# Optimization experiments

Hardware: AMD Instinct MI355X
Metric: run time of the kernel (lower is better)

## Reference

```python
import jax, jax.numpy as jnp
import numpy as np
import math

B, S, D = 2, 2048, 1024
H, HD = 16, 64
ROT = 16          # rotary_dim = head_dim * 0.25
FF = 4096
EPS = 1e-5


def setup_inputs() -> dict:
    key = jax.random.key(0)
    ks = jax.random.split(key, 12)
    sc = lambda *sh: 0.02
    inp = {
        "x": jax.random.normal(ks[0], (B, S, D), jnp.float32),
        "attention_mask": jnp.tril(jnp.ones((S, S), bool))[None, None],  # causal [1,1,S,S]
        "W_qkv": jax.random.normal(ks[1], (3 * D, D), jnp.float32) * 0.02,
        "b_qkv": jnp.zeros((3 * D,), jnp.float32),
        "W_o": jax.random.normal(ks[2], (D, D), jnp.float32) * 0.02,
        "b_o": jnp.zeros((D,), jnp.float32),
        "ln1_w": jnp.ones((D,), jnp.float32),
        "ln1_b": jnp.zeros((D,), jnp.float32),
        "ln2_w": jnp.ones((D,), jnp.float32),
        "ln2_b": jnp.zeros((D,), jnp.float32),
        "W1": jax.random.normal(ks[3], (FF, D), jnp.float32) * 0.02,
        "b1": jnp.zeros((FF,), jnp.float32),
        "W2": jax.random.normal(ks[4], (D, FF), jnp.float32) * 0.02,
        "b2": jnp.zeros((D,), jnp.float32),
    }
    # real rotary frequencies, shaped [1,1,S,ROT//2,2]
    inv_freq = 1.0 / (10000.0 ** (jnp.arange(0, ROT, 2, dtype=jnp.float32) / ROT))
    t = jnp.arange(S, dtype=jnp.float32)
    ang = t[:, None] * inv_freq[None, :]                      # [S, ROT//2]
    inp["freqs_cis"] = jnp.stack([jnp.cos(ang), jnp.sin(ang)], -1)[None, None]
    return inp


def layer_norm(x, w, b):
    mu = jnp.mean(x, -1, keepdims=True)
    var = jnp.mean(jnp.square(x - mu), -1, keepdims=True)
    return (x - mu) * jax.lax.rsqrt(var + EPS) * w + b


def apply_rotate_emb(x, freqs_cis):
    # x: [B,H,S,ROT]; freqs_cis: [1,1,S,ROT//2,2]
    x1, x2 = x[..., : ROT // 2], x[..., ROT // 2 :]
    cos, sin = freqs_cis[..., 0], freqs_cis[..., 1]
    return jnp.concatenate([x1 * cos - x2 * sin, x1 * sin + x2 * cos], -1)


def reference(x, attention_mask, freqs_cis, W_qkv, b_qkv, W_o, b_o,
              ln1_w, ln1_b, ln2_w, ln2_b, W1, b1, W2, b2):
    h = layer_norm(x, ln1_w, ln1_b)
    qkv = jnp.einsum("bsd,ed->bse", h, W_qkv) + b_qkv
    q, k, v = jnp.split(qkv, 3, axis=-1)
    to_heads = lambda t: t.reshape(B, S, H, HD).transpose(0, 2, 1, 3)  # [B,H,S,HD]
    q, k, v = to_heads(q), to_heads(k), to_heads(v)
    q = jnp.concatenate([apply_rotate_emb(q[..., :ROT], freqs_cis), q[..., ROT:]], -1)
    k = jnp.concatenate([apply_rotate_emb(k[..., :ROT], freqs_cis), k[..., ROT:]], -1)
    scores = jnp.einsum("bhqd,bhkd->bhqk", q, k) / math.sqrt(HD)
    scores = jnp.where(attention_mask, scores, -jnp.inf)
    probs = jax.nn.softmax(scores, axis=-1)
    out = jnp.einsum("bhqk,bhkd->bhqd", probs, v)
    out = out.transpose(0, 2, 1, 3).reshape(B, S, D)
    attn_out = jnp.einsum("bsd,ed->bse", out, W_o) + b_o
    # parallel residual (dropout is identity in eval)
    h2 = layer_norm(x, ln2_w, ln2_b)
    ff = jnp.einsum("bsf,df->bsd", jax.nn.gelu(jnp.einsum("bsd,fd->bsf", h2, W1) + b1, approximate=False), W2) + b2
    return x + ff + attn_out
```

## Files before the change

kernel.cpp:

```cpp
#include <hip/hip_runtime.h>

#define DEV __device__ __forceinline__

typedef __bf16 bf16;
typedef bf16 bf16x4 __attribute__((ext_vector_type(4)));
typedef bf16 bf16x8 __attribute__((ext_vector_type(8)));
typedef float f32x4 __attribute__((ext_vector_type(4)));

DEV f32x4 mfma16(bf16x8 a, bf16x8 b, f32x4 c) {
  return __builtin_amdgcn_mfma_f32_16x16x32_bf16(a, b, c, 0, 0, 0);
}

DEV void gload_lds16(const bf16* g, bf16* l) {
  __builtin_amdgcn_global_load_lds((const __attribute__((address_space(1))) void*)g,
                                   (__attribute__((address_space(3))) void*)l, 16, 0, 0);
}

#define PH_BAR __builtin_amdgcn_s_barrier()
#define VM(NSTR) asm volatile("s_waitcnt vmcnt(" NSTR ")" ::: "memory")
#define WAITBAR(NSTR) asm volatile("s_waitcnt vmcnt(" NSTR ")\n\ts_barrier" ::: "memory")

DEV float fast_gelu(float x) {
  const float z = x * x;
  const float w = __builtin_fmaf(z, 0.1029353f, 2.3019853f);
  const float e = __builtin_amdgcn_exp2f(x * w);
  const float r = __builtin_amdgcn_rcpf(1.0f + e);
  return x - x * r;
}

__global__ __launch_bounds__(256) void ln_cast_all(
    const float* __restrict__ x,
    const float* __restrict__ ln1w, const float* __restrict__ ln1b,
    const float* __restrict__ ln2w, const float* __restrict__ ln2b,
    bf16* __restrict__ h1, bf16* __restrict__ h2,
    const float* __restrict__ Wqkv_f, const float* __restrict__ W1_f,
    const float* __restrict__ Wo_f, const float* __restrict__ W2_f,
    bf16* __restrict__ wQKV, bf16* __restrict__ w1, bf16* __restrict__ wCat)
{
  const int b = blockIdx.x, t = threadIdx.x;
  if (b < 4096) {
    __shared__ float red[2][4];
    const int lane = t & 63, wave = t >> 6;
    const float4 v = ((const float4*)(x + (size_t)b * 1024))[t];
    float vv[4] = {v.x, v.y, v.z, v.w};
    float s = vv[0] + vv[1] + vv[2] + vv[3];
    float q = vv[0]*vv[0] + vv[1]*vv[1] + vv[2]*vv[2] + vv[3]*vv[3];
    #pragma unroll
    for (int o = 32; o; o >>= 1) { s += __shfl_xor(s, o); q += __shfl_xor(q, o); }
    if (lane == 0) { red[0][wave] = s; red[1][wave] = q; }
    __syncthreads();
    s = red[0][0] + red[0][1] + red[0][2] + red[0][3];
    q = red[1][0] + red[1][1] + red[1][2] + red[1][3];
    const float mu = s * (1.0f / 1024.0f);
    const float var = q * (1.0f / 1024.0f) - mu * mu;
    const float rs = rsqrtf(var + 1e-5f);
    bf16x4 o1, o2;
    #pragma unroll
    for (int j = 0; j < 4; ++j) {
      const int i = t * 4 + j;
      const float xh = (vv[j] - mu) * rs;
      o1[j] = (bf16)(xh * ln1w[i] + ln1b[i]);
      o2[j] = (bf16)(xh * ln2w[i] + ln2b[i]);
    }
    *(bf16x4*)&h1[(size_t)b * 1024 + t * 4] = o1;
    *(bf16x4*)&h2[(size_t)b * 1024 + t * 4] = o2;
    return;
  }
  const int cb = b - 4096;
  if (cb < 3072) {
    const int i = cb * 256 + t;
    const float4 v = ((const float4*)Wqkv_f)[i];
    bf16x4 o = {(bf16)v.x, (bf16)v.y, (bf16)v.z, (bf16)v.w};
    ((bf16x4*)wQKV)[i] = o;
  } else if (cb < 7168) {
    const int i = (cb - 3072) * 256 + t;
    const float4 v = ((const float4*)W1_f)[i];
    bf16x4 o = {(bf16)v.x, (bf16)v.y, (bf16)v.z, (bf16)v.w};
    ((bf16x4*)w1)[i] = o;
  } else if (cb < 8192) {
    const int row = cb - 7168;
    const float4 v = *(const float4*)&Wo_f[(size_t)row * 1024 + t * 4];
    bf16x4 o = {(bf16)v.x, (bf16)v.y, (bf16)v.z, (bf16)v.w};
    *(bf16x4*)&wCat[(size_t)row * 5120 + t * 4] = o;
  } else {
    const int row = cb - 8192;
    #pragma unroll
    for (int k = 0; k < 4; ++k) {
      const int col = t * 4 + k * 1024;
      const float4 v = *(const float4*)&W2_f[(size_t)row * 4096 + col];
      bf16x4 o = {(bf16)v.x, (bf16)v.y, (bf16)v.z, (bf16)v.w};
      *(bf16x4*)&wCat[(size_t)row * 5120 + 1024 + col] = o;
    }
  }
}

DEV bf16x8 ldfrag(const bf16* unit, int lr, int g) {
  return *(const bf16x8*)&unit[lr * 32 + ((g ^ ((lr >> 1) & 3)) << 3)];
}
DEV void read_bfr(const bf16* unit, int blr, int g, bf16x8 bfr[4]) {
  #pragma unroll
  for (int nj = 0; nj < 4; ++nj) bfr[nj] = ldfrag(unit, blr + nj * 16, g);
}
DEV void read_af(const bf16* unit, int alr, int g, bf16x8 af[4]) {
  #pragma unroll
  for (int ml = 0; ml < 4; ++ml) af[ml] = ldfrag(unit, alr + ml * 16, g);
}
DEV void do_mfma(const bf16x8 af[4], const bf16x8 bfr[4], f32x4 acc[8][4], int mh) {
  __builtin_amdgcn_s_setprio(1);
  #pragma unroll
  for (int ml = 0; ml < 4; ++ml)
    #pragma unroll
    for (int nj = 0; nj < 4; ++nj)
      acc[mh * 4 + ml][nj] = mfma16(af[ml], bfr[nj], acc[mh * 4 + ml][nj]);
  __builtin_amdgcn_s_setprio(0);
}

DEV void gemm_kloop(bf16 (*As)[2][2][4096], bf16 (*Bs)[2][2][4096],
                    const bf16* aU[2][2], const bf16* bU[2][2],
                    int wave, int alr, int blr, int bub, int g, int nkt,
                    f32x4 acc[8][4])
{
  bf16x8 bfr[4], af[4];
#define STG_A(bf_, kkh_, ub_, ko_) gload_lds16(aU[kkh_][ub_] + (ko_), &As[bf_][kkh_][ub_][wave * 512])
#define STG_B(bf_, kkh_, ub_, ko_) gload_lds16(bU[kkh_][ub_] + (ko_), &Bs[bf_][kkh_][ub_][wave * 512])
  STG_B(0, 0, 0, 0); STG_B(0, 0, 1, 0); STG_A(0, 0, 0, 0); STG_A(0, 0, 1, 0);
  STG_B(0, 1, 0, 0); STG_B(0, 1, 1, 0); STG_A(0, 1, 0, 0); STG_A(0, 1, 1, 0);
  WAITBAR("4");

  for (int t = 0; t < nkt - 1; ++t) {
    const int buf = t & 1, nxt = buf ^ 1;
    const int ko = (t + 1) * 64;
    read_bfr(&Bs[buf][0][bub][0], blr, g, bfr);
    read_af(&As[buf][0][0][0], alr, g, af);
    STG_B(nxt, 0, 0, ko); STG_B(nxt, 0, 1, ko);
    PH_BAR;
    do_mfma(af, bfr, acc, 0);
    PH_BAR;
    read_af(&As[buf][0][1][0], alr, g, af);
    STG_A(nxt, 0, 0, ko); STG_A(nxt, 0, 1, ko);
    PH_BAR;
    do_mfma(af, bfr, acc, 1);
    VM("4");
    PH_BAR;
    read_bfr(&Bs[buf][1][bub][0], blr, g, bfr);
    read_af(&As[buf][1][0][0], alr, g, af);
    STG_B(nxt, 1, 0, ko); STG_B(nxt, 1, 1, ko);
    PH_BAR;
    do_mfma(af, bfr, acc, 0);
    PH_BAR;
    read_af(&As[buf][1][1][0], alr, g, af);
    STG_A(nxt, 1, 0, ko); STG_A(nxt, 1, 1, ko);
    PH_BAR;
    do_mfma(af, bfr, acc, 1);
    VM("4");
    PH_BAR;
  }
  {
    const int buf = (nkt - 1) & 1;
    read_bfr(&Bs[buf][0][bub][0], blr, g, bfr);
    read_af(&As[buf][0][0][0], alr, g, af);
    PH_BAR;
    do_mfma(af, bfr, acc, 0);
    PH_BAR;
    read_af(&As[buf][0][1][0], alr, g, af);
    PH_BAR;
    do_mfma(af, bfr, acc, 1);
    VM("0");
    PH_BAR;
    read_bfr(&Bs[buf][1][bub][0], blr, g, bfr);
    read_af(&As[buf][1][0][0], alr, g, af);
    PH_BAR;
    do_mfma(af, bfr, acc, 0);
    PH_BAR;
    read_af(&As[buf][1][1][0], alr, g, af);
    PH_BAR;
    do_mfma(af, bfr, acc, 1);
  }
#undef STG_A
#undef STG_B
}

template <int EPI>
__global__ __launch_bounds__(512) void gemm256(
    const bf16* __restrict__ A, const bf16* __restrict__ B,
    const float* __restrict__ bias, void* __restrict__ Cv,
    void* __restrict__ P1, void* __restrict__ P2, void* __restrict__ P3,
    int K, int ldc, int ntiles, int nbx, int nkt)
{
  __shared__ __align__(16) bf16 As[2][2][2][4096];
  __shared__ __align__(16) bf16 Bs[2][2][2][4096];
  const int tid = threadIdx.x;
  const int lane = tid & 63, wave = tid >> 6;
  const int wm = wave >> 2, wn = wave & 3;
  const int g = lane >> 4, c = lane & 15;
  const int cpx = gridDim.x >> 3;
  const int swz = ((int)blockIdx.x & 7) * cpx + ((int)blockIdx.x >> 3);
  const int tile = swz % ntiles;
  const int sk = swz / ntiles;
  const int bm = (tile / nbx) * 256, bn = (tile % nbx) * 256;

  const int slr = tid >> 2;
  const int sch = (tid & 3) ^ ((tid >> 3) & 3);
  const bf16* aU[2][2];
  const bf16* bU[2][2];
  {
    const bf16* a0 = A + (size_t)(bm + ((slr >> 6) * 128) + (slr & 63)) * K
                       + (size_t)sk * nkt * 64 + sch * 8;
    const bf16* b0 = B + (size_t)(bn + slr) * K + (size_t)sk * nkt * 64 + sch * 8;
    aU[0][0] = a0;            aU[0][1] = a0 + (size_t)64 * K;
    aU[1][0] = a0 + 32;       aU[1][1] = a0 + (size_t)64 * K + 32;
    bU[0][0] = b0;            bU[0][1] = b0 + (size_t)128 * K;
    bU[1][0] = b0 + 32;       bU[1][1] = b0 + (size_t)128 * K + 32;
  }

  f32x4 acc[8][4] = {};
  const int alr = (wm << 6) + c;
  const int blr = ((wn & 1) << 6) + c;
  const int bub = wn >> 1;

  gemm_kloop(As, Bs, aU, bU, wave, alr, blr, bub, g, nkt, acc);

  bf16* Pp = nullptr;
  if constexpr (EPI == 2)
    Pp = (bf16*)((sk == 1) ? P1 : (sk == 2) ? P2 : (sk == 3) ? P3 : Cv);
  const int row0 = bm + wm * 128 + 4 * g;
  const int col0 = bn + wn * 64 + c;
  #pragma unroll
  for (int mi = 0; mi < 8; ++mi) {
    #pragma unroll
    for (int nj = 0; nj < 4; ++nj) {
      const int col = col0 + nj * 16;
      float bv = 0.0f;
      if constexpr (EPI < 2) bv = bias[col];
      #pragma unroll
      for (int r = 0; r < 4; ++r) {
        const size_t idx = (size_t)(row0 + mi * 16 + r) * ldc + col;
        float vo = acc[mi][nj][r] + bv;
        if constexpr (EPI == 0) {
          ((bf16*)Cv)[idx] = (bf16)vo;
        } else if constexpr (EPI == 1) {
          ((bf16*)Cv)[idx] = (bf16)fast_gelu(vo);
        } else {
          Pp[idx] = (bf16)vo;
        }
      }
    }
  }
}

__global__ __launch_bounds__(256) void combine_out(
    const bf16* __restrict__ q0, const bf16* __restrict__ q1,
    const bf16* __restrict__ q2, const bf16* __restrict__ q3,
    const float* __restrict__ x,
    const float* __restrict__ bo, const float* __restrict__ b2,
    float* __restrict__ out)
{
  const int row = blockIdx.x, t = threadIdx.x;
  const size_t base = (size_t)row * 1024 + t * 4;
  const bf16x4 a0 = *(const bf16x4*)&q0[base];
  const bf16x4 a1 = *(const bf16x4*)&q1[base];
  const bf16x4 a2 = *(const bf16x4*)&q2[base];
  const bf16x4 a3 = *(const bf16x4*)&q3[base];
  const float4 vx = *(const float4*)&x[base];
  const float4 vb = *(const float4*)&bo[t * 4];
  const float4 vc = *(const float4*)&b2[t * 4];
  float4 o;
  o.x = (float)a0[0] + (float)a1[0] + (float)a2[0] + (float)a3[0] + vx.x + vb.x + vc.x;
  o.y = (float)a0[1] + (float)a1[1] + (float)a2[1] + (float)a3[1] + vx.y + vb.y + vc.y;
  o.z = (float)a0[2] + (float)a1[2] + (float)a2[2] + (float)a3[2] + vx.z + vb.z + vc.z;
  o.w = (float)a0[3] + (float)a1[3] + (float)a2[3] + (float)a3[3] + vx.w + vb.w + vc.w;
  *(float4*)&out[base] = o;
}

__global__ __launch_bounds__(256) void rope_reshape(
    const bf16* __restrict__ qkv, const float* __restrict__ freqs,
    bf16* __restrict__ Q, bf16* __restrict__ K, bf16* __restrict__ VT)
{
  __shared__ bf16 vt[64][72];
  const int t = threadIdx.x;
  const int bh = blockIdx.y, b = bh >> 4, h = bh & 15;
  const int sc = blockIdx.x * 64;
  const int sl = t >> 2, s = sc + sl;
  const int d0 = (t & 3) * 16;

  const size_t rowbase = (size_t)(b * 2048 + s) * 3072 + h * 64 + d0;
  const size_t obase = ((size_t)bh * 2048 + s) * 64 + d0;

  #pragma unroll
  for (int which = 0; which < 2; ++which) {
    const bf16* src = qkv + rowbase + which * 1024;
    bf16x8 v0 = *(const bf16x8*)src;
    bf16x8 v1 = *(const bf16x8*)(src + 8);
    if (d0 == 0) {
      bf16x8 r0, r1;
      #pragma unroll
      for (int j = 0; j < 8; ++j) {
        const float cs = freqs[s * 16 + j * 2];
        const float sn = freqs[s * 16 + j * 2 + 1];
        const float x1 = (float)v0[j], x2 = (float)v1[j];
        r0[j] = (bf16)(x1 * cs - x2 * sn);
        r1[j] = (bf16)(x1 * sn + x2 * cs);
      }
      v0 = r0; v1 = r1;
    }
    bf16* dst = (which == 0 ? Q : K) + obase;
    *(bf16x8*)dst = v0;
    *(bf16x8*)(dst + 8) = v1;
  }
  {
    const bf16* src = qkv + rowbase + 2048;
    bf16x8 v0 = *(const bf16x8*)src;
    bf16x8 v1 = *(const bf16x8*)(src + 8);
    #pragma unroll
    for (int j = 0; j < 8; ++j) { vt[sl][d0 + j] = v0[j]; vt[sl][d0 + 8 + j] = v1[j]; }
  }
  __syncthreads();
  {
    const int d = t >> 2;
    const int s0 = (t & 3) * 16;
    bf16x8 o0, o1;
    #pragma unroll
    for (int j = 0; j < 8; ++j) { o0[j] = vt[s0 + j][d]; o1[j] = vt[s0 + 8 + j][d]; }
    bf16* dst = VT + ((size_t)bh * 64 + d) * 2048 + sc + s0;
    *(bf16x8*)dst = o0;
    *(bf16x8*)(dst + 8) = o1;
  }
}

__global__ __launch_bounds__(512, 4) void attn_kernel(
    const bf16* __restrict__ Q, const bf16* __restrict__ Kg,
    const bf16* __restrict__ VTg, bf16* __restrict__ O, int ldO)
{
  __shared__ __align__(16) bf16 Ks[4][64][64];
  __shared__ __align__(16) bf16 Vs[4][64][64];
  __shared__ __align__(16) bf16 Ps[8][16][64];

  const int tid = threadIdx.x;
  const int lane = tid & 63, wave = tid >> 6;
  const int g = lane >> 4, c = lane & 15;
  const int L = blockIdx.x;
  const int heavy = (L < 256);
  const int r = heavy ? L : (L - 256);
  const int bh = r >> 3;
  const int qtile = heavy ? (8 + (r & 7)) : (7 - (r & 7));
  const int qw = qtile * 128 + wave * 16;

  const bf16* Qp = Q + (size_t)bh * 2048 * 64;
  const bf16* Kp = Kg + (size_t)bh * 2048 * 64;
  const bf16* Vp = VTg + (size_t)bh * 64 * 2048;

  const int srow = lane >> 3;
  const int schunk = (lane & 7) ^ srow;
  const int svr = wave * 8 + srow;
  const size_t kdelta = (size_t)64 * 64;

  bf16x8 qreg[2];
  {
    const float qs = 0.125f * 1.44269504f;
    bf16x8 t0 = *(const bf16x8*)&Qp[(size_t)(qw + c) * 64 + g * 8];
    bf16x8 t1 = *(const bf16x8*)&Qp[(size_t)(qw + c) * 64 + 32 + g * 8];
    #pragma unroll
    for (int j = 0; j < 8; ++j) {
      qreg[0][j] = (bf16)((float)t0[j] * qs);
      qreg[1][j] = (bf16)((float)t1[j] * qs);
    }
  }
  bf16x8 ones;
  #pragma unroll
  for (int j = 0; j < 8; ++j) ones[j] = (bf16)1.0f;

  const int cq = c & 7;
  int fo[4][2];
  #pragma unroll
  for (int i = 0; i < 4; ++i)
    #pragma unroll
    for (int kk = 0; kk < 2; ++kk)
      fo[i][kk] = (i * 16 + c) * 64 + (((kk * 4 + g) ^ cq) << 3);
  bf16* pw[4];
  #pragma unroll
  for (int kf = 0; kf < 4; ++kf)
    pw[kf] = &Ps[wave][c][((((kf * 2 + (g >> 1)) ^ cq) << 3)) + ((g & 1) << 2)];
  const bf16* pr[2];
  #pragma unroll
  for (int kk = 0; kk < 2; ++kk)
    pr[kk] = &Ps[wave][c][((kk * 4 + g) ^ cq) << 3];
  const bf16* ks0 = &Ks[0][0][0];
  const bf16* vs0 = &Vs[0][0][0];

  f32x4 oacc[4] = {};
  f32x4 lacc = {};
  float m_ = -1e30f;

  const int nkb = 2 * qtile + 2;
#define STAGE(j_) do { const int b4_ = (j_) & 3;                                     \
    gload_lds16(&Kp[(size_t)((j_) * 64 + svr) * 64 + schunk * 8], &Ks[b4_][wave * 8][0]); \
    gload_lds16(&Vp[(size_t)svr * 2048 + (j_) * 64 + schunk * 8], &Vs[b4_][wave * 8][0]); \
  } while (0)

  auto qkt = [&](f32x4* st, int bufi) {
    const bf16* kt = ks0 + bufi * kdelta;
    __builtin_amdgcn_s_setprio(1);
    #pragma unroll
    for (int kf = 0; kf < 4; ++kf) {
      f32x4 z = {};
      z = mfma16(*(const bf16x8*)(kt + fo[kf][0]), qreg[0], z);
      st[kf] = mfma16(*(const bf16x8*)(kt + fo[kf][1]), qreg[1], z);
    }
    __builtin_amdgcn_s_setprio(0);
  };

  auto smpv = [&](const f32x4* st, int j_, int bufi) {
    const int kbase = j_ * 64;
    float v[16];
    if (kbase + 63 > qw) {
      const int qrel = qw + c - kbase;
      #pragma unroll
      for (int kf = 0; kf < 4; ++kf)
        #pragma unroll
        for (int rr = 0; rr < 4; ++rr)
          v[kf * 4 + rr] = (kf * 16 + 4 * g + rr <= qrel) ? st[kf][rr] : -1e30f;
    } else {
      #pragma unroll
      for (int kf = 0; kf < 4; ++kf)
        #pragma unroll
        for (int rr = 0; rr < 4; ++rr)
          v[kf * 4 + rr] = st[kf][rr];
    }
    float u0 = fmaxf(fmaxf(v[0], v[1]), v[2]);
    float u1 = fmaxf(fmaxf(v[3], v[4]), v[5]);
    float u2 = fmaxf(fmaxf(v[6], v[7]), v[8]);
    float u3 = fmaxf(fmaxf(v[9], v[10]), v[11]);
    float u4 = fmaxf(fmaxf(v[12], v[13]), v[14]);
    float tm = fmaxf(fmaxf(fmaxf(u0, u1), u2), fmaxf(fmaxf(u3, u4), v[15]));
    if (__any(tm > m_ + 8.0f)) {
      float tr = fmaxf(tm, __shfl_xor(tm, 16));
      tr = fmaxf(tr, __shfl_xor(tr, 32));
      const float mn = fmaxf(m_, tr);
      const float alpha = __builtin_amdgcn_exp2f(m_ - mn);
      m_ = mn;
      lacc[0] *= alpha; lacc[1] *= alpha; lacc[2] *= alpha; lacc[3] *= alpha;
      #pragma unroll
      for (int df = 0; df < 4; ++df) {
        oacc[df][0] *= alpha; oacc[df][1] *= alpha;
        oacc[df][2] *= alpha; oacc[df][3] *= alpha;
      }
    }
    bf16 pq[16];
    #pragma unroll
    for (int i = 0; i < 16; ++i)
      pq[i] = (bf16)__builtin_amdgcn_exp2f(v[i] - m_);
    #pragma unroll
    for (int kf = 0; kf < 4; ++kf) {
      bf16x4 pk = {pq[kf * 4], pq[kf * 4 + 1], pq[kf * 4 + 2], pq[kf * 4 + 3]};
      *(bf16x4*)pw[kf] = pk;
    }
    bf16x8 pfrag0 = *(const bf16x8*)pr[0];
    bf16x8 pfrag1 = *(const bf16x8*)pr[1];
    const bf16* vt = vs0 + bufi * kdelta;
    __builtin_amdgcn_s_setprio(1);
    #pragma unroll
    for (int df = 0; df < 4; ++df) {
      oacc[df] = mfma16(*(const bf16x8*)(vt + fo[df][0]), pfrag0, oacc[df]);
      oacc[df] = mfma16(*(const bf16x8*)(vt + fo[df][1]), pfrag1, oacc[df]);
    }
    lacc = mfma16(ones, pfrag0, lacc);
    lacc = mfma16(ones, pfrag1, lacc);
    __builtin_amdgcn_s_setprio(0);
  };

  f32x4 stA[4], stB[4];
  STAGE(0); STAGE(1); STAGE(2);
  VM("2");
  PH_BAR;
  qkt(stA, 0);

  const int nit = nkb >> 1;
  for (int i = 0; i < nit; ++i) {
    const int jA = 2 * i, jB = 2 * i + 1;
    const bool stgA = (jA + 3 < nkb);
    if (stgA) STAGE(jA + 3);
    if (jB * 64 <= qw + 15) qkt(stB, jB & 3);
    smpv(stA, jA, jA & 3);
    if (stgA) { VM("2"); } else { VM("0"); }
    PH_BAR;
    const bool stgB = (jB + 3 < nkb);
    if (stgB) STAGE(jB + 3);
    if (jB + 1 < nkb && (jB + 1) * 64 <= qw + 15) qkt(stA, (jB + 1) & 3);
    if (jB * 64 <= qw + 15) smpv(stB, jB, jB & 3);
    if (stgB) { VM("2"); } else { VM("0"); }
    PH_BAR;
  }
#undef STAGE

  const int b = bh >> 4, h = bh & 15;
  const float inv = 1.0f / lacc[0];
  const int s = qw + c;
  #pragma unroll
  for (int df = 0; df < 4; ++df) {
    bf16x4 o;
    #pragma unroll
    for (int rr = 0; rr < 4; ++rr) o[rr] = (bf16)(oacc[df][rr] * inv);
    *(bf16x4*)&O[(size_t)(b * 2048 + s) * ldO + h * 64 + df * 16 + 4 * g] = o;
  }
}

extern "C" void kernel_launch(void* const* d_in, const int* in_sizes, int n_in,
                              void* d_out, int out_size, void* d_ws, size_t ws_size,
                              hipStream_t stream) {
  const float* x     = (const float*)d_in[0];
  const float* W_qkv = (const float*)d_in[2];
  const float* b_qkv = (const float*)d_in[3];
  const float* W_o   = (const float*)d_in[4];
  const float* b_o   = (const float*)d_in[5];
  const float* ln1w  = (const float*)d_in[6];
  const float* ln1b  = (const float*)d_in[7];
  const float* ln2w  = (const float*)d_in[8];
  const float* ln2b  = (const float*)d_in[9];
  const float* W1    = (const float*)d_in[10];
  const float* b1    = (const float*)d_in[11];
  const float* W2    = (const float*)d_in[12];
  const float* b2    = (const float*)d_in[13];
  const float* freqs = (const float*)d_in[14];
  float* out = (float*)d_out;

  char* ws = (char*)d_ws;
  const size_t MB = (size_t)1 << 20;
  bf16* h1   = (bf16*)(ws + 0 * MB);
  bf16* h2   = (bf16*)(ws + 8 * MB);
  bf16* wQKV = (bf16*)(ws + 16 * MB);
  bf16* wCat = (bf16*)(ws + 22 * MB);
  bf16* w1   = (bf16*)(ws + 32 * MB);
  bf16* qkv  = (bf16*)(ws + 40 * MB);
  bf16* Qb   = (bf16*)(ws + 64 * MB);
  bf16* Kb   = (bf16*)(ws + 72 * MB);
  bf16* VTb  = (bf16*)(ws + 80 * MB);
  bf16* A2   = (bf16*)(ws + 88 * MB);
  bf16* q0   = (bf16*)(ws + 0 * MB);
  bf16* q1   = (bf16*)(ws + 8 * MB);
  bf16* q2   = (bf16*)(ws + 40 * MB);
  bf16* q3   = (bf16*)(ws + 48 * MB);

  ln_cast_all<<<13312, 256, 0, stream>>>(x, ln1w, ln1b, ln2w, ln2b, h1, h2,
                                         W_qkv, W1, W_o, W2, wQKV, w1, wCat);
  gemm256<0><<<192, 512, 0, stream>>>(h1, wQKV, b_qkv, qkv,
                                      nullptr, nullptr, nullptr,
                                      1024, 3072, 192, 12, 16);
  rope_reshape<<<dim3(32, 32), 256, 0, stream>>>(qkv, freqs, Qb, Kb, VTb);
  attn_kernel<<<512, 512, 0, stream>>>(Qb, Kb, VTb, A2, 5120);
  gemm256<1><<<256, 512, 0, stream>>>(h2, w1, b1, A2 + 1024,
                                      nullptr, nullptr, nullptr,
                                      1024, 5120, 256, 16, 16);
  gemm256<2><<<256, 512, 0, stream>>>(A2, wCat, nullptr, q0,
                                      q1, q2, q3,
                                      5120, 1024, 64, 4, 20);
  combine_out<<<4096, 256, 0, stream>>>(q0, q1, q2, q3, x, b_o, b2, out);
}
```

Baseline: 195.4 us.

## Fuse RoPE, head reshape and V transpose into QKV GEMM epilogue; unroll attention loop

The QKV GEMM gains a new epilogue that applies rotary embedding through lane shuffles, pre-scales Q by the softmax scale and log2e, and writes Q/K in head-major layout and V transposed. This drops the separate rope_reshape kernel and its round trip through the qkv buffer. The attention kernel no longer rescales Q on load, and its main loop is unrolled by four with compile-time LDS buffer indices to cut address arithmetic. The tradeoff is scattered, narrow global stores in the GEMM epilogue (2-byte Q/K stores and strided VT stores) in place of the old kernel's vectorized writes.

```diff
diff --git a/kernel.cpp b/kernel.cpp
--- a/kernel.cpp
+++ b/kernel.cpp
@@ -185,6 +185,7 @@
     const bf16* __restrict__ A, const bf16* __restrict__ B,
     const float* __restrict__ bias, void* __restrict__ Cv,
     void* __restrict__ P1, void* __restrict__ P2, void* __restrict__ P3,
+    const float* __restrict__ freqs,
     int K, int ldc, int ntiles, int nbx, int nkt)
 {
   __shared__ __align__(16) bf16 As[2][2][2][4096];
@@ -220,11 +221,54 @@
 
   gemm_kloop(As, Bs, aU, bU, wave, alr, blr, bub, g, nkt, acc);
 
+  const int row0 = bm + wm * 128 + 4 * g;
+  const int col0 = bn + wn * 64 + c;
+
+  if constexpr (EPI == 3) {
+    bf16* Qb  = (bf16*)Cv;
+    bf16* Kb  = (bf16*)P1;
+    bf16* VTb = (bf16*)P2;
+    const int which = bn >> 10;
+    const int h = ((bn & 1023) >> 6) + wn;
+    #pragma unroll
+    for (int mi = 0; mi < 8; ++mi) {
+      const int srow = row0 + mi * 16;
+      const int bb = srow >> 11, sl0 = srow & 2047;
+      #pragma unroll
+      for (int nj = 0; nj < 4; ++nj) {
+        const int d = nj * 16 + c;
+        const float bv = bias[bn + wn * 64 + d];
+        float vo[4];
+        #pragma unroll
+        for (int r = 0; r < 4; ++r) vo[r] = acc[mi][nj][r] + bv;
+        if (which == 2) {
+          bf16x4 o = {(bf16)vo[0], (bf16)vo[1], (bf16)vo[2], (bf16)vo[3]};
+          *(bf16x4*)&VTb[((size_t)(bb * 16 + h) * 64 + d) * 2048 + sl0] = o;
+        } else {
+          if (nj == 0) {
+            #pragma unroll
+            for (int r = 0; r < 4; ++r) {
+              const int sl = sl0 + r;
+              const float cs = freqs[sl * 16 + (c & 7) * 2];
+              const float sn = freqs[sl * 16 + (c & 7) * 2 + 1];
+              const float p = __shfl_xor(vo[r], 8);
+              vo[r] = (c < 8) ? (vo[r] * cs - p * sn) : (p * sn + vo[r] * cs);
+            }
+          }
+          bf16* dst = (which == 0) ? Qb : Kb;
+          const float sc = (which == 0) ? 0.18033688f  : 1.0f;
+          #pragma unroll
+          for (int r = 0; r < 4; ++r)
+            dst[((size_t)(bb * 16 + h) * 2048 + (sl0 + r)) * 64 + d] = (bf16)(vo[r] * sc);
+        }
+      }
+    }
+    return;
+  }
+
   bf16* Pp = nullptr;
   if constexpr (EPI == 2)
     Pp = (bf16*)((sk == 1) ? P1 : (sk == 2) ? P2 : (sk == 3) ? P3 : Cv);
-  const int row0 = bm + wm * 128 + 4 * g;
-  const int col0 = bn + wn * 64 + c;
   #pragma unroll
   for (int mi = 0; mi < 8; ++mi) {
     #pragma unroll
@@ -272,61 +316,6 @@
   *(float4*)&out[base] = o;
 }
 
-__global__ __launch_bounds__(256) void rope_reshape(
-    const bf16* __restrict__ qkv, const float* __restrict__ freqs,
-    bf16* __restrict__ Q, bf16* __restrict__ K, bf16* __restrict__ VT)
-{
-  __shared__ bf16 vt[64][72];
-  const int t = threadIdx.x;
-  const int bh = blockIdx.y, b = bh >> 4, h = bh & 15;
-  const int sc = blockIdx.x * 64;
-  const int sl = t >> 2, s = sc + sl;
-  const int d0 = (t & 3) * 16;
-
-  const size_t rowbase = (size_t)(b * 2048 + s) * 3072 + h * 64 + d0;
-  const size_t obase = ((size_t)bh * 2048 + s) * 64 + d0;
-
-  #pragma unroll
-  for (int which = 0; which < 2; ++which) {
-    const bf16* src = qkv + rowbase + which * 1024;
-    bf16x8 v0 = *(const bf16x8*)src;
-    bf16x8 v1 = *(const bf16x8*)(src + 8);
-    if (d0 == 0) {
-      bf16x8 r0, r1;
-      #pragma unroll
-      for (int j = 0; j < 8; ++j) {
-        const float cs = freqs[s * 16 + j * 2];
-        const float sn = freqs[s * 16 + j * 2 + 1];
-        const float x1 = (float)v0[j], x2 = (float)v1[j];
-        r0[j] = (bf16)(x1 * cs - x2 * sn);
-        r1[j] = (bf16)(x1 * sn + x2 * cs);
-      }
-      v0 = r0; v1 = r1;
-    }
-    bf16* dst = (which == 0 ? Q : K) + obase;
-    *(bf16x8*)dst = v0;
-    *(bf16x8*)(dst + 8) = v1;
-  }
-  {
-    const bf16* src = qkv + rowbase + 2048;
-    bf16x8 v0 = *(const bf16x8*)src;
-    bf16x8 v1 = *(const bf16x8*)(src + 8);
-    #pragma unroll
-    for (int j = 0; j < 8; ++j) { vt[sl][d0 + j] = v0[j]; vt[sl][d0 + 8 + j] = v1[j]; }
-  }
-  __syncthreads();
-  {
-    const int d = t >> 2;
-    const int s0 = (t & 3) * 16;
-    bf16x8 o0, o1;
-    #pragma unroll
-    for (int j = 0; j < 8; ++j) { o0[j] = vt[s0 + j][d]; o1[j] = vt[s0 + 8 + j][d]; }
-    bf16* dst = VT + ((size_t)bh * 64 + d) * 2048 + sc + s0;
-    *(bf16x8*)dst = o0;
-    *(bf16x8*)(dst + 8) = o1;
-  }
-}
-
 __global__ __launch_bounds__(512, 4) void attn_kernel(
     const bf16* __restrict__ Q, const bf16* __restrict__ Kg,
     const bf16* __restrict__ VTg, bf16* __restrict__ O, int ldO)
@@ -352,19 +341,10 @@
   const int srow = lane >> 3;
   const int schunk = (lane & 7) ^ srow;
   const int svr = wave * 8 + srow;
-  const size_t kdelta = (size_t)64 * 64;
 
   bf16x8 qreg[2];
-  {
-    const float qs = 0.125f * 1.44269504f;
-    bf16x8 t0 = *(const bf16x8*)&Qp[(size_t)(qw + c) * 64 + g * 8];
-    bf16x8 t1 = *(const bf16x8*)&Qp[(size_t)(qw + c) * 64 + 32 + g * 8];
-    #pragma unroll
-    for (int j = 0; j < 8; ++j) {
-      qreg[0][j] = (bf16)((float)t0[j] * qs);
-      qreg[1][j] = (bf16)((float)t1[j] * qs);
-    }
-  }
+  qreg[0] = *(const bf16x8*)&Qp[(size_t)(qw + c) * 64 + g * 8];
+  qreg[1] = *(const bf16x8*)&Qp[(size_t)(qw + c) * 64 + 32 + g * 8];
   bf16x8 ones;
   #pragma unroll
   for (int j = 0; j < 8; ++j) ones[j] = (bf16)1.0f;
@@ -384,21 +364,23 @@
   #pragma unroll
   for (int kk = 0; kk < 2; ++kk)
     pr[kk] = &Ps[wave][c][((kk * 4 + g) ^ cq) << 3];
-  const bf16* ks0 = &Ks[0][0][0];
-  const bf16* vs0 = &Vs[0][0][0];
+
+  bf16* const kdst[4] = {&Ks[0][0][0] + wave * 512, &Ks[1][0][0] + wave * 512,
+                         &Ks[2][0][0] + wave * 512, &Ks[3][0][0] + wave * 512};
+  bf16* const vdst[4] = {&Vs[0][0][0] + wave * 512, &Vs[1][0][0] + wave * 512,
+                         &Vs[2][0][0] + wave * 512, &Vs[3][0][0] + wave * 512};
 
   f32x4 oacc[4] = {};
   f32x4 lacc = {};
   float m_ = -1e30f;
 
   const int nkb = 2 * qtile + 2;
-#define STAGE(j_) do { const int b4_ = (j_) & 3;                                     \
-    gload_lds16(&Kp[(size_t)((j_) * 64 + svr) * 64 + schunk * 8], &Ks[b4_][wave * 8][0]); \
-    gload_lds16(&Vp[(size_t)svr * 2048 + (j_) * 64 + schunk * 8], &Vs[b4_][wave * 8][0]); \
+#define STAGE(j_, B4_) do {                                                         \
+    gload_lds16(&Kp[(size_t)((j_) * 64 + svr) * 64 + schunk * 8], kdst[B4_]);       \
+    gload_lds16(&Vp[(size_t)svr * 2048 + (j_) * 64 + schunk * 8], vdst[B4_]);       \
   } while (0)
 
-  auto qkt = [&](f32x4* st, int bufi) {
-    const bf16* kt = ks0 + bufi * kdelta;
+  auto qkt = [&](f32x4* st, const bf16* kt) {
     __builtin_amdgcn_s_setprio(1);
     #pragma unroll
     for (int kf = 0; kf < 4; ++kf) {
@@ -409,7 +391,7 @@
     __builtin_amdgcn_s_setprio(0);
   };
 
-  auto smpv = [&](const f32x4* st, int j_, int bufi) {
+  auto smpv = [&](const f32x4* st, int j_, const bf16* vt) {
     const int kbase = j_ * 64;
     float v[16];
     if (kbase + 63 > qw) {
@@ -456,7 +438,6 @@
     }
     bf16x8 pfrag0 = *(const bf16x8*)pr[0];
     bf16x8 pfrag1 = *(const bf16x8*)pr[1];
-    const bf16* vt = vs0 + bufi * kdelta;
     __builtin_amdgcn_s_setprio(1);
     #pragma unroll
     for (int df = 0; df < 4; ++df) {
@@ -468,28 +449,35 @@
     __builtin_amdgcn_s_setprio(0);
   };
 
+#define ABODY(j_, BUF, stC, stN) do {                                          \
+    const bool stg_ = ((j_) + 3 < nkb);                                        \
+    if (stg_) STAGE((j_) + 3, (((BUF) + 3) & 3));                              \
+    if (((j_) + 1) < nkb && ((j_) + 1) * 64 <= qw + 15)                        \
+      qkt(stN, &Ks[((BUF) + 1) & 3][0][0]);                                    \
+    if ((j_) * 64 <= qw + 15) smpv(stC, (j_), &Vs[(BUF)][0][0]);               \
+    if (stg_) { VM("2"); } else { VM("0"); }                                   \
+    PH_BAR;                                                                    \
+  } while (0)
+
   f32x4 stA[4], stB[4];
-  STAGE(0); STAGE(1); STAGE(2);
+  STAGE(0, 0); STAGE(1, 1); STAGE(2, 2);
   VM("2");
   PH_BAR;
-  qkt(stA, 0);
-
-  const int nit = nkb >> 1;
-  for (int i = 0; i < nit; ++i) {
-    const int jA = 2 * i, jB = 2 * i + 1;
-    const bool stgA = (jA + 3 < nkb);
-    if (stgA) STAGE(jA + 3);
-    if (jB * 64 <= qw + 15) qkt(stB, jB & 3);
-    smpv(stA, jA, jA & 3);
-    if (stgA) { VM("2"); } else { VM("0"); }
-    PH_BAR;
-    const bool stgB = (jB + 3 < nkb);
-    if (stgB) STAGE(jB + 3);
-    if (jB + 1 < nkb && (jB + 1) * 64 <= qw + 15) qkt(stA, (jB + 1) & 3);
-    if (jB * 64 <= qw + 15) smpv(stB, jB, jB & 3);
-    if (stgB) { VM("2"); } else { VM("0"); }
-    PH_BAR;
-  }
+  qkt(stA, &Ks[0][0][0]);
+
+  const int nq = nkb >> 2;
+  for (int qd = 0; qd < nq; ++qd) {
+    const int j0 = 4 * qd;
+    ABODY(j0 + 0, 0, stA, stB);
+    ABODY(j0 + 1, 1, stB, stA);
+    ABODY(j0 + 2, 2, stA, stB);
+    ABODY(j0 + 3, 3, stB, stA);
+  }
+  if (nkb & 2) {
+    ABODY(nkb - 2, 0, stA, stB);
+    ABODY(nkb - 1, 1, stB, stA);
+  }
+#undef ABODY
 #undef STAGE
 
   const int b = bh >> 4, h = bh & 15;
@@ -530,7 +518,6 @@
   bf16* wQKV = (bf16*)(ws + 16 * MB);
   bf16* wCat = (bf16*)(ws + 22 * MB);
   bf16* w1   = (bf16*)(ws + 32 * MB);
-  bf16* qkv  = (bf16*)(ws + 40 * MB);
   bf16* Qb   = (bf16*)(ws + 64 * MB);
   bf16* Kb   = (bf16*)(ws + 72 * MB);
   bf16* VTb  = (bf16*)(ws + 80 * MB);
@@ -542,16 +529,15 @@
 
   ln_cast_all<<<13312, 256, 0, stream>>>(x, ln1w, ln1b, ln2w, ln2b, h1, h2,
                                          W_qkv, W1, W_o, W2, wQKV, w1, wCat);
-  gemm256<0><<<192, 512, 0, stream>>>(h1, wQKV, b_qkv, qkv,
-                                      nullptr, nullptr, nullptr,
+  gemm256<3><<<192, 512, 0, stream>>>(h1, wQKV, b_qkv, Qb,
+                                      Kb, VTb, nullptr, freqs,
                                       1024, 3072, 192, 12, 16);
-  rope_reshape<<<dim3(32, 32), 256, 0, stream>>>(qkv, freqs, Qb, Kb, VTb);
   attn_kernel<<<512, 512, 0, stream>>>(Qb, Kb, VTb, A2, 5120);
   gemm256<1><<<256, 512, 0, stream>>>(h2, w1, b1, A2 + 1024,
-                                      nullptr, nullptr, nullptr,
+                                      nullptr, nullptr, nullptr, nullptr,
                                       1024, 5120, 256, 16, 16);
   gemm256<2><<<256, 512, 0, stream>>>(A2, wCat, nullptr, q0,
-                                      q1, q2, q3,
+                                      q1, q2, q3, nullptr,
                                       5120, 1024, 64, 4, 20);
   combine_out<<<4096, 256, 0, stream>>>(q0, q1, q2, q3, x, b_o, b2, out);
 }
```

After: 186.4 us. -4.6%, faster.
